# Kernel tuning notes

Hardware: AMD Instinct MI355X
Metric: run time of the kernel (lower is better)

The kernel has to match this reference:

```python
import jax, jax.numpy as jnp
import numpy as np
import math

B, T, D, H = 4, 2048, 1024, 16
DH = D // H

def setup_inputs() -> dict:
    key = jax.random.key(0)
    ks = jax.random.split(key, 5)
    scale = 1.0 / math.sqrt(D)
    x = jax.random.normal(ks[0], (B, T, D), dtype=jnp.float32)
    Wq = jax.random.normal(ks[1], (D, D), dtype=jnp.float32) * scale
    Wk = jax.random.normal(ks[2], (D, D), dtype=jnp.float32) * scale
    Wv = jax.random.normal(ks[3], (D, D), dtype=jnp.float32) * scale
    Wo = jax.random.normal(ks[4], (D, D), dtype=jnp.float32) * scale
    mask = jnp.tril(jnp.ones((T, T), dtype=jnp.int32))  # causal, 1=keep
    return {"x": x, "mask": mask, "Wq": Wq, "Wk": Wk, "Wv": Wv, "Wo": Wo}

def reference(x, mask, Wq, Wk, Wv, Wo):
    Bx, Tx, Dx = x.shape
    # nn.Linear(bias=False): y = x @ W.T
    q = (x @ Wq.T).reshape(Bx, Tx, H, DH).transpose(0, 2, 1, 3)  # [B,H,T,dh]
    k = (x @ Wk.T).reshape(Bx, Tx, H, DH).transpose(0, 2, 1, 3)
    v = (x @ Wv.T).reshape(Bx, Tx, H, DH).transpose(0, 2, 1, 3)
    scores = jnp.einsum('bhqd,bhkd->bhqk', q, k) / math.sqrt(DH)
    m = mask[None, None, :, :]  # [1,1,T,T]
    scores = scores + (m == 0).astype(scores.dtype) * -1e9
    attn = jax.nn.softmax(scores, axis=-1)  # stable (max-subtract) like original
    out = jnp.einsum('bhqk,bhkd->bhqd', attn, v)
    out = out.transpose(0, 2, 1, 3).reshape(Bx, Tx, Dx)
    return out @ Wo.T
```

## Files before the change

kernel.cpp:

```cpp
#include <hip/hip_runtime.h>
#include <stdint.h>

#define B_  4
#define T_  2048
#define D_  1024
#define H_  16
#define DH_ 64

typedef unsigned short u16;
typedef __attribute__((ext_vector_type(8))) short bf16x8;
typedef __attribute__((ext_vector_type(8))) unsigned short u16x8;
typedef __attribute__((ext_vector_type(4))) unsigned short u16x4;
typedef __attribute__((ext_vector_type(4))) float f32x4;

#define NT_ ((size_t)B_ * T_ * D_)
#define QSCALE 0.18033688011112043f

__device__ __forceinline__ u16 f2bf(float f) {
    union { float f; uint32_t u; } v; v.f = f;
    uint32_t r = v.u + 0x7FFFu + ((v.u >> 16) & 1u);
    return (u16)(r >> 16);
}

__device__ __forceinline__ uint32_t pack2(float lo, float hi) {
    union { float f; uint32_t u; } a, b; a.f = lo; b.f = hi;
    return __builtin_amdgcn_perm(b.u, a.u, 0x07060302u);
}

__device__ __forceinline__ void gl2lds16(const u16* g, u16* l) {
    __builtin_amdgcn_global_load_lds(
        (const __attribute__((address_space(1))) unsigned int*)g,
        (__attribute__((address_space(3))) unsigned int*)l,
        16, 0, 0);
}

#define VMCNT(n) asm volatile("s_waitcnt vmcnt(" #n ")" ::: "memory")
#define LGKM0()  asm volatile("s_waitcnt lgkmcnt(0)" ::: "memory")
#define SB0()    __builtin_amdgcn_sched_barrier(0)

__device__ __forceinline__ bf16x8 ldsrd(const u16* base, int row, int ks,
                                        int lq, int swzr) {
    int off = row * 128 + ks * 64 + lq * 16;
    return *(const bf16x8*)((const char*)base + (off ^ swzr));
}

__global__ __launch_bounds__(256) void cvt_x_kernel(
    const float* __restrict__ src, u16* __restrict__ dst, int n8)
{
    int i = blockIdx.x * 256 + threadIdx.x;
    if (i >= n8) return;
    f32x4 a = ((const f32x4*)src)[2 * i];
    f32x4 b = ((const f32x4*)src)[2 * i + 1];
    u16x8 o;
    o[0]=f2bf(a[0]); o[1]=f2bf(a[1]); o[2]=f2bf(a[2]); o[3]=f2bf(a[3]);
    o[4]=f2bf(b[0]); o[5]=f2bf(b[1]); o[6]=f2bf(b[2]); o[7]=f2bf(b[3]);
    ((u16x8*)dst)[i] = o;
}

__global__ __launch_bounds__(256) void cvt_w_kernel(
    const float* __restrict__ w0, const float* __restrict__ w1,
    const float* __restrict__ w2, const float* __restrict__ w3,
    u16* __restrict__ dst)
{
    const float* src = (blockIdx.y == 0) ? w0 : (blockIdx.y == 1) ? w1
                     : (blockIdx.y == 2) ? w2 : w3;
    u16* d = dst + (size_t)blockIdx.y * (D_ * D_);
    int i = blockIdx.x * 256 + threadIdx.x;
    f32x4 a = ((const f32x4*)src)[2 * i];
    f32x4 b = ((const f32x4*)src)[2 * i + 1];
    u16x8 o;
    o[0]=f2bf(a[0]); o[1]=f2bf(a[1]); o[2]=f2bf(a[2]); o[3]=f2bf(a[3]);
    o[4]=f2bf(b[0]); o[5]=f2bf(b[1]); o[6]=f2bf(b[2]); o[7]=f2bf(b[3]);
    ((u16x8*)d)[i] = o;
}

template<int OUT_MODE>
__global__ __launch_bounds__(512) void gemm8_kernel(
    const u16* __restrict__ X, const u16* __restrict__ W,
    void* __restrict__ C, int M, int N, int K)
{
    __shared__ __align__(16) u16 Ab2[2][256 * 64];
    __shared__ __align__(16) u16 Bb2[2][192 * 64];

    const int tid  = threadIdx.x;
    const int wave = tid >> 6;
    const int lane = tid & 63;
    const int lq = lane >> 4, lm = lane & 15;
    const int wm = wave >> 2;
    const int wn = wave & 3;

    const int xcd = (int)blockIdx.x & 7;
    const int idx = (int)blockIdx.x >> 3;
    const int m0 = (((xcd & 3) << 3) + (idx & 7)) << 8;
    const int n0 = (((xcd >> 2) << 3) + (idx >> 3)) * 192;

    const int srow = wave * 8 + (lane >> 3);
    const int scol = ((lane & 7) ^ (lane >> 3)) << 3;
    const u16* gA = X + (size_t)(m0 + srow) * K + scol;
    const u16* gB = W + (size_t)(n0 + srow) * K + scol;
    const size_t rK64 = (size_t)64 * K;

    const int swzr = (lm & 7) << 4;

    f32x4 acc[8][3] = {};
    const int NT = K >> 6;

    gl2lds16(gA,            (u16*)Ab2[0] + wave * 512);
    gl2lds16(gA + rK64,     (u16*)Ab2[0] + 4096  + wave * 512);
    gl2lds16(gA + 2 * rK64, (u16*)Ab2[0] + 8192  + wave * 512);
    gl2lds16(gA + 3 * rK64, (u16*)Ab2[0] + 12288 + wave * 512);
    gl2lds16(gB,            (u16*)Bb2[0] + wave * 512);
    gl2lds16(gB + rK64,     (u16*)Bb2[0] + 4096  + wave * 512);
    gl2lds16(gB + 2 * rK64, (u16*)Bb2[0] + 8192  + wave * 512);
    gl2lds16(gB + 64,            (u16*)Bb2[1] + wave * 512);
    gl2lds16(gB + 64 + rK64,     (u16*)Bb2[1] + 4096  + wave * 512);
    gl2lds16(gB + 64 + 2 * rK64, (u16*)Bb2[1] + 8192  + wave * 512);
    VMCNT(3);
    __builtin_amdgcn_s_barrier();

#define MFMA_HALF(IOFF)                                                     \
        __builtin_amdgcn_s_setprio(1);                                      \
        _Pragma("unroll")                                                   \
        for (int ks = 0; ks < 2; ++ks)                                      \
            _Pragma("unroll")                                               \
            for (int i4 = 0; i4 < 4; ++i4)                                  \
                _Pragma("unroll")                                           \
                for (int j = 0; j < 3; ++j)                                 \
                    acc[(IOFF) + i4][j] =                                   \
                        __builtin_amdgcn_mfma_f32_16x16x32_bf16(            \
                            af[i4][ks], bq[j][ks], acc[(IOFF) + i4][j],     \
                            0, 0, 0);                                       \
        __builtin_amdgcn_s_setprio(0);

#pragma unroll 1
    for (int t = 0; t < NT; ++t) {
        const u16* Ac = Ab2[t & 1];
        const u16* Bc = Bb2[t & 1];
        u16* Abn = (u16*)Ab2[(t + 1) & 1];
        u16* Bbc = (u16*)Bb2[t & 1];
        const bool stA = (t + 1 < NT);
        const bool stB = (t + 2 < NT);
        const u16* gAs = gA + (size_t)(t + 1) * 64;
        const u16* gBs = gB + (size_t)(t + 2) * 64;

        bf16x8 af[4][2], bq[3][2];

#pragma unroll
        for (int i4 = 0; i4 < 4; ++i4)
#pragma unroll
            for (int ks = 0; ks < 2; ++ks)
                af[i4][ks] = ldsrd(Ac, wm * 128 + i4 * 16 + lm, ks, lq, swzr);
#pragma unroll
        for (int j = 0; j < 3; ++j)
#pragma unroll
            for (int ks = 0; ks < 2; ++ks)
                bq[j][ks] = ldsrd(Bc, wn * 48 + j * 16 + lm, ks, lq, swzr);
        if (stA) {
            gl2lds16(gAs,        Abn + wave * 512);
            gl2lds16(gAs + rK64, Abn + 4096 + wave * 512);
        }
        SB0(); __builtin_amdgcn_s_barrier();
        LGKM0(); SB0();
        MFMA_HALF(0)
        SB0(); __builtin_amdgcn_s_barrier();

#pragma unroll
        for (int i4 = 0; i4 < 4; ++i4)
#pragma unroll
            for (int ks = 0; ks < 2; ++ks)
                af[i4][ks] = ldsrd(Ac, wm * 128 + (4 + i4) * 16 + lm, ks, lq, swzr);
        if (stA) {
            gl2lds16(gAs + 2 * rK64, Abn + 8192  + wave * 512);
            gl2lds16(gAs + 3 * rK64, Abn + 12288 + wave * 512);
        }
        if (stB) {
            gl2lds16(gBs,            Bbc + wave * 512);
            gl2lds16(gBs + rK64,     Bbc + 4096 + wave * 512);
            gl2lds16(gBs + 2 * rK64, Bbc + 8192 + wave * 512);
        }
        SB0(); __builtin_amdgcn_s_barrier();
        LGKM0(); SB0();
        MFMA_HALF(4)
        SB0();
        if (stB)      { VMCNT(3); }
        else if (stA) { VMCNT(0); }
        __builtin_amdgcn_s_barrier();
    }
#undef MFMA_HALF

#pragma unroll
    for (int i = 0; i < 8; ++i)
#pragma unroll
        for (int j = 0; j < 3; ++j) {
            int rowb = m0 + wm * 128 + i * 16 + lq * 4;
            int col  = n0 + wn * 48 + j * 16 + lm;
            if (OUT_MODE == 2) {
#pragma unroll
                for (int r = 0; r < 4; ++r)
                    ((float*)C)[(size_t)(rowb + r) * N + col] = acc[i][j][r];
            } else {
                u16* Qp = (u16*)C;
                int region = col >> 10;
                int colr = col & 1023;
                if (region == 0) {
#pragma unroll
                    for (int r = 0; r < 4; ++r)
                        Qp[(size_t)(rowb + r) * D_ + colr] = f2bf(acc[i][j][r] * QSCALE);
                } else if (region == 1) {
#pragma unroll
                    for (int r = 0; r < 4; ++r)
                        (Qp + NT_)[(size_t)(rowb + r) * D_ + colr] = f2bf(acc[i][j][r]);
                } else {
                    int b = rowb >> 11, tt2 = rowb & (T_ - 1);
                    u16x4 pk;
#pragma unroll
                    for (int r = 0; r < 4; ++r) pk[r] = f2bf(acc[i][j][r]);
                    *(u16x4*)((Qp + 2 * NT_) + ((size_t)b * D_ + colr) * T_ + tt2) = pk;
                }
            }
        }
}

__global__ __launch_bounds__(512) void gemm8o_kernel(
    const u16* __restrict__ X, const u16* __restrict__ W,
    float* __restrict__ C)
{
    __shared__ __align__(16) u16 Ab2[2][256 * 64];
    __shared__ __align__(16) u16 Bb2[2][128 * 64];

    const int K = 1024, N = 1024;
    const int tid  = threadIdx.x;
    const int wave = tid >> 6;
    const int lane = tid & 63;
    const int lq = lane >> 4, lm = lane & 15;
    const int wm = wave >> 2;
    const int wn = wave & 3;

    const int xcd = (int)blockIdx.x & 7;
    const int idx = (int)blockIdx.x >> 3;
    const int m0 = (((xcd & 3) << 3) + (idx & 7)) << 8;
    const int n0 = (((xcd >> 2) << 2) + (idx >> 3)) << 7;

    const int srow = wave * 8 + (lane >> 3);
    const int scol = ((lane & 7) ^ (lane >> 3)) << 3;
    const u16* gA = X + (size_t)(m0 + srow) * K + scol;
    const u16* gB = W + (size_t)(n0 + srow) * K + scol;
    const size_t rK64 = (size_t)64 * K;

    const int swzr = (lm & 7) << 4;

    f32x4 acc[8][2] = {};
    bf16x8 afA[2][2], afB[2][2];
    bf16x8 bqA[2][2], bqB[2][2];
    const int NT = 16;

    gl2lds16(gA,            (u16*)Ab2[0] + wave * 512);
    gl2lds16(gA + rK64,     (u16*)Ab2[0] + 4096  + wave * 512);
    gl2lds16(gA + 2 * rK64, (u16*)Ab2[0] + 8192  + wave * 512);
    gl2lds16(gA + 3 * rK64, (u16*)Ab2[0] + 12288 + wave * 512);
    gl2lds16(gB,            (u16*)Bb2[0] + wave * 512);
    gl2lds16(gB + rK64,     (u16*)Bb2[0] + 4096  + wave * 512);
    gl2lds16(gB + 64,            (u16*)Bb2[1] + wave * 512);
    gl2lds16(gB + 64 + rK64,     (u16*)Bb2[1] + 4096  + wave * 512);
    VMCNT(2);
    __builtin_amdgcn_s_barrier();
#pragma unroll
    for (int i2 = 0; i2 < 2; ++i2)
#pragma unroll
        for (int ks = 0; ks < 2; ++ks)
            afA[i2][ks] = ldsrd(Ab2[0], wm * 128 + i2 * 16 + lm, ks, lq, swzr);
#pragma unroll
    for (int j = 0; j < 2; ++j)
#pragma unroll
        for (int ks = 0; ks < 2; ++ks)
            bqA[j][ks] = ldsrd(Bb2[0], wn * 32 + j * 16 + lm, ks, lq, swzr);

    auto tile_body = [&](int t, bf16x8 (&bqU)[2][2], bf16x8 (&bqF)[2][2])
        __attribute__((always_inline)) -> void {
        const u16* Ac = Ab2[t & 1];
        const u16* An = Ab2[(t + 1) & 1];
        const u16* Bn = Bb2[(t + 1) & 1];
        u16* Abn = (u16*)Ab2[(t + 1) & 1];
        u16* Bbc = (u16*)Bb2[t & 1];
        const bool stA = (t + 1 < NT);
        const bool stB = (t + 2 < NT);
        const u16* gAs = gA + (size_t)(t + 1) * 64;
        const u16* gBs = gB + (size_t)(t + 2) * 64;

#define MFMA_PHO(Q, AF, BQ)                                                 \
        __builtin_amdgcn_s_setprio(1);                                      \
        _Pragma("unroll")                                                   \
        for (int ks = 0; ks < 2; ++ks)                                      \
            _Pragma("unroll")                                               \
            for (int i2 = 0; i2 < 2; ++i2)                                  \
                _Pragma("unroll")                                           \
                for (int j = 0; j < 2; ++j)                                 \
                    acc[2 * (Q) + i2][j] =                                  \
                        __builtin_amdgcn_mfma_f32_16x16x32_bf16(            \
                            AF[i2][ks], BQ[j][ks], acc[2 * (Q) + i2][j],    \
                            0, 0, 0);                                       \
        __builtin_amdgcn_s_setprio(0);

#define RD_AFO(SET, P, BASE)                                                \
        _Pragma("unroll")                                                   \
        for (int i2 = 0; i2 < 2; ++i2)                                      \
            _Pragma("unroll")                                               \
            for (int ks = 0; ks < 2; ++ks)                                  \
                SET[i2][ks] = ldsrd(BASE,                                   \
                    wm * 128 + (2 * (P) + i2) * 16 + lm, ks, lq, swzr);

        RD_AFO(afB, 1, Ac);
        if (stA) {
            gl2lds16(gAs,        Abn + wave * 512);
            gl2lds16(gAs + rK64, Abn + 4096 + wave * 512);
        }
        SB0(); __builtin_amdgcn_s_barrier(); SB0();
        MFMA_PHO(0, afA, bqU); SB0();
        __builtin_amdgcn_s_barrier();

        RD_AFO(afA, 2, Ac);
        if (stA) {
            gl2lds16(gAs + 2 * rK64, Abn + 8192  + wave * 512);
            gl2lds16(gAs + 3 * rK64, Abn + 12288 + wave * 512);
        }
        SB0(); __builtin_amdgcn_s_barrier(); SB0();
        MFMA_PHO(1, afB, bqU); SB0();
        __builtin_amdgcn_s_barrier();

        RD_AFO(afB, 3, Ac);
        if (stB)
            gl2lds16(gBs, Bbc + wave * 512);
        SB0(); __builtin_amdgcn_s_barrier(); SB0();
        MFMA_PHO(2, afA, bqU); SB0();
        if (stB)      { VMCNT(1); }
        else if (stA) { VMCNT(0); }
        __builtin_amdgcn_s_barrier();

        if (stA) {
            RD_AFO(afA, 0, An);
#pragma unroll
            for (int j = 0; j < 2; ++j)
#pragma unroll
                for (int ks = 0; ks < 2; ++ks)
                    bqF[j][ks] = ldsrd(Bn, wn * 32 + j * 16 + lm, ks, lq, swzr);
        }
        if (stB)
            gl2lds16(gBs + rK64, Bbc + 4096 + wave * 512);
        SB0(); __builtin_amdgcn_s_barrier(); SB0();
        MFMA_PHO(3, afB, bqU); SB0();
        __builtin_amdgcn_s_barrier();
#undef RD_AFO
#undef MFMA_PHO
    };

#pragma unroll 1
    for (int tt = 0; tt < NT; tt += 2) {
        tile_body(tt,     bqA, bqB);
        tile_body(tt + 1, bqB, bqA);
    }

#pragma unroll
    for (int i = 0; i < 8; ++i)
#pragma unroll
        for (int j = 0; j < 2; ++j) {
            int rowb = m0 + wm * 128 + i * 16 + lq * 4;
            int col  = n0 + wn * 32 + j * 16 + lm;
#pragma unroll
            for (int r = 0; r < 4; ++r)
                C[(size_t)(rowb + r) * N + col] = acc[i][j][r];
        }
}

__global__ __launch_bounds__(128) void attn_kernel(
    const u16* __restrict__ Qg, const u16* __restrict__ Kg,
    const u16* __restrict__ Vtg, u16* __restrict__ Og)
{
    __shared__ __align__(16) u16 Pl[2 * 64 * 40];

    const int tid  = threadIdx.x;
    const int wave = tid >> 6;
    const int lane = tid & 63;
    const int lq = lane >> 4, lm = lane & 15;
    const int id = blockIdx.x;
    const int xs = id & 7;
    const int bh = xs + 8 * ((id >> 3) & 7);
    const int qj = 31 - (id >> 6);
    const int b = bh >> 4, h = bh & 15;

    const size_t batchoff = (size_t)b * T_ * D_;
    const size_t headoff  = (size_t)h * DH_;
    const size_t vbase    = (size_t)bh * DH_ * T_;

    u16* pw = Pl + wave * 64 * 40;

    const int qw  = qj * 64;
    const int ktd = qj >> 1;
    const int odd = qj & 1;

    bf16x8 aq[4][2];
#pragma unroll
    for (int qf = 0; qf < 4; ++qf) {
        const u16* qrow = Qg + batchoff + (size_t)(qw + qf * 16 + lm) * D_ + headoff;
        aq[qf][0] = *(const bf16x8*)(qrow + lq * 8);
        aq[qf][1] = *(const bf16x8*)(qrow + 32 + lq * 8);
    }

    f32x4 oaccT[4][4] = {};
    float l_lane[4] = {0.f, 0.f, 0.f, 0.f};

#pragma unroll 1
    for (int kt = wave; kt <= ktd; kt += 2) {
        const bool diag = (kt == ktd);
        const int ksmax = diag ? (odd ? 3 : 1) : 3;

#pragma unroll
        for (int c = 0; c < 4; ++c) {
            if (c <= ksmax) {
#pragma unroll
                for (int t = 0; t < 2; ++t) {
                    const int mt = 2 * c + t;
                    const u16* krow = Kg + batchoff
                        + (size_t)(kt * 128 + mt * 16 + lm) * D_ + headoff;
                    bf16x8 kf0 = *(const bf16x8*)(krow + lq * 8);
                    bf16x8 kf1 = *(const bf16x8*)(krow + 32 + lq * 8);
                    f32x4 s[4];
                    __builtin_amdgcn_s_setprio(1);
#pragma unroll
                    for (int qf = 0; qf < 4; ++qf) {
                        s[qf] = f32x4{0.f, 0.f, 0.f, 0.f};
                        s[qf] = __builtin_amdgcn_mfma_f32_16x16x32_bf16(
                            kf0, aq[qf][0], s[qf], 0, 0, 0);
                        s[qf] = __builtin_amdgcn_mfma_f32_16x16x32_bf16(
                            kf1, aq[qf][1], s[qf], 0, 0, 0);
                    }
                    __builtin_amdgcn_s_setprio(0);
                    if (diag) {
                        int keyb = kt * 128 + mt * 16 + lq * 4;
#pragma unroll
                        for (int qf = 0; qf < 4; ++qf) {
                            int query = qw + qf * 16 + lm;
#pragma unroll
                            for (int r = 0; r < 4; ++r)
                                if (keyb + r > query) s[qf][r] = -1e9f;
                        }
                    }
#pragma unroll
                    for (int qf = 0; qf < 4; ++qf) {
                        float p0 = __builtin_amdgcn_exp2f(s[qf][0]);
                        float p1 = __builtin_amdgcn_exp2f(s[qf][1]);
                        float p2 = __builtin_amdgcn_exp2f(s[qf][2]);
                        float p3 = __builtin_amdgcn_exp2f(s[qf][3]);
                        l_lane[qf] += (p0 + p1) + (p2 + p3);
                        uint2 d; d.x = pack2(p0, p1); d.y = pack2(p2, p3);
                        *(uint2*)(pw + (qf * 16 + lm) * 40 + t * 16 + lq * 4) = d;
                    }
                }

                bf16x8 pf[4];
#pragma unroll
                for (int qf = 0; qf < 4; ++qf)
                    pf[qf] = *(const bf16x8*)(pw + (qf * 16 + lm) * 40 + lq * 8);
                __builtin_amdgcn_s_setprio(1);
#pragma unroll
                for (int mo = 0; mo < 4; ++mo) {
                    const u16* vrow = Vtg + vbase
                        + (size_t)(mo * 16 + lm) * T_ + kt * 128 + c * 32;
                    bf16x8 vf = *(const bf16x8*)(vrow + lq * 8);
#pragma unroll
                    for (int qf = 0; qf < 4; ++qf)
                        oaccT[qf][mo] = __builtin_amdgcn_mfma_f32_16x16x32_bf16(
                            vf, pf[qf], oaccT[qf][mo], 0, 0, 0);
                }
                __builtin_amdgcn_s_setprio(0);
            }
        }
    }

    float* Cf = (float*)Pl;
    const int cswz = (lane ^ (lane >> 3)) * 4;
    __syncthreads();
    if (wave == 1) {
#pragma unroll
        for (int qf = 0; qf < 2; ++qf)
#pragma unroll
            for (int mo = 0; mo < 4; ++mo)
                *(f32x4*)&Cf[(qf * 4 + mo) * 256 + cswz] = oaccT[qf][mo];
#pragma unroll
        for (int qf = 0; qf < 4; ++qf)
            Cf[2048 + qf * 64 + lane] = l_lane[qf];
    }
    __syncthreads();
    if (wave == 0) {
#pragma unroll
        for (int qf = 0; qf < 2; ++qf)
#pragma unroll
            for (int mo = 0; mo < 4; ++mo) {
                f32x4 o = *(const f32x4*)&Cf[(qf * 4 + mo) * 256 + cswz];
#pragma unroll
                for (int r = 0; r < 4; ++r) oaccT[qf][mo][r] += o[r];
            }
#pragma unroll
        for (int qf = 0; qf < 4; ++qf) l_lane[qf] += Cf[2048 + qf * 64 + lane];
    }
    __syncthreads();
    if (wave == 1) {
#pragma unroll
        for (int qf = 2; qf < 4; ++qf)
#pragma unroll
            for (int mo = 0; mo < 4; ++mo)
                *(f32x4*)&Cf[((qf - 2) * 4 + mo) * 256 + cswz] = oaccT[qf][mo];
    }
    __syncthreads();
    if (wave == 0) {
#pragma unroll
        for (int qf = 2; qf < 4; ++qf)
#pragma unroll
            for (int mo = 0; mo < 4; ++mo) {
                f32x4 o = *(const f32x4*)&Cf[((qf - 2) * 4 + mo) * 256 + cswz];
#pragma unroll
                for (int r = 0; r < 4; ++r) oaccT[qf][mo][r] += o[r];
            }
#pragma unroll
        for (int qf = 0; qf < 4; ++qf) {
            float l = l_lane[qf];
            l += __shfl_xor(l, 16, 64);
            l += __shfl_xor(l, 32, 64);
            float inv = 1.0f / l;
            int row = qw + qf * 16 + lm;
            u16* obase = Og + batchoff + (size_t)row * D_ + headoff;
#pragma unroll
            for (int mo = 0; mo < 4; ++mo) {
                uint2 d;
                d.x = pack2(oaccT[qf][mo][0] * inv, oaccT[qf][mo][1] * inv);
                d.y = pack2(oaccT[qf][mo][2] * inv, oaccT[qf][mo][3] * inv);
                *(uint2*)(obase + mo * 16 + lq * 4) = d;
            }
        }
    }
}

extern "C" void kernel_launch(void* const* d_in, const int* in_sizes, int n_in,
                              void* d_out, int out_size, void* d_ws, size_t ws_size,
                              hipStream_t stream)
{
    const float* x  = (const float*)d_in[0];
    const float* Wq = (const float*)d_in[2];
    const float* Wk = (const float*)d_in[3];
    const float* Wv = (const float*)d_in[4];
    const float* Wo = (const float*)d_in[5];

    const size_t DD = (size_t)D_ * D_;
    u16* Qb  = (u16*)d_ws;
    u16* Kb  = Qb + NT_;
    u16* Vb  = Kb + NT_;
    u16* Ob  = Vb + NT_;
    u16* xb  = Ob + NT_;
    u16* wb  = xb + NT_;

    const int M = B_ * T_;

    cvt_x_kernel<<<dim3((int)(NT_ / 8 / 256)), 256, 0, stream>>>(x, xb, (int)(NT_ / 8));
    cvt_w_kernel<<<dim3((int)(DD / 8 / 256), 4), 256, 0, stream>>>(Wq, Wk, Wv, Wo, wb);

    gemm8_kernel<3><<<dim3((M / 256) * (3 * D_ / 192)), 512, 0, stream>>>(
        xb, wb, Qb, M, 3 * D_, D_);

    attn_kernel<<<dim3(2048), 128, 0, stream>>>(Qb, Kb, Vb, Ob);

    gemm8o_kernel<<<dim3(256), 512, 0, stream>>>(Ob, wb + 3 * DD, (float*)d_out);
}
```

Baseline: 268.8 us.

## Merge GEMM K-step halves into one phase with triple-buffered B tiles

The projection GEMM main loop used to split each 64-wide K tile into two halves, each with its own LDS reads, global-to-LDS prefetches and block barrier. It now reads all eight A fragments at once, issues every A and B prefetch together, and runs all 48 MFMAs in one burst, leaving a single barrier per iteration. The B tile buffer becomes a three-slot ring, so the tile two steps ahead can be loaded without overwriting the one being read. The aim is to halve barrier stalls per K step. In exchange it uses more LDS and more VGPRs for the A fragments, and it overlaps LDS reads with MFMAs less finely.

Measured after the change: 267.4 us. About the same (-0.5%).

```diff
diff --git a/kernel.cpp b/kernel.cpp
--- a/kernel.cpp
+++ b/kernel.cpp
@@ -80,7 +80,7 @@
     void* __restrict__ C, int M, int N, int K)
 {
     __shared__ __align__(16) u16 Ab2[2][256 * 64];
-    __shared__ __align__(16) u16 Bb2[2][192 * 64];
+    __shared__ __align__(16) u16 Bb3[3][192 * 64];
 
     const int tid  = threadIdx.x;
     const int wave = tid >> 6;
@@ -109,84 +109,68 @@
     gl2lds16(gA + rK64,     (u16*)Ab2[0] + 4096  + wave * 512);
     gl2lds16(gA + 2 * rK64, (u16*)Ab2[0] + 8192  + wave * 512);
     gl2lds16(gA + 3 * rK64, (u16*)Ab2[0] + 12288 + wave * 512);
-    gl2lds16(gB,            (u16*)Bb2[0] + wave * 512);
-    gl2lds16(gB + rK64,     (u16*)Bb2[0] + 4096  + wave * 512);
-    gl2lds16(gB + 2 * rK64, (u16*)Bb2[0] + 8192  + wave * 512);
-    gl2lds16(gB + 64,            (u16*)Bb2[1] + wave * 512);
-    gl2lds16(gB + 64 + rK64,     (u16*)Bb2[1] + 4096  + wave * 512);
-    gl2lds16(gB + 64 + 2 * rK64, (u16*)Bb2[1] + 8192  + wave * 512);
+    gl2lds16(gB,            (u16*)Bb3[0] + wave * 512);
+    gl2lds16(gB + rK64,     (u16*)Bb3[0] + 4096  + wave * 512);
+    gl2lds16(gB + 2 * rK64, (u16*)Bb3[0] + 8192  + wave * 512);
+    gl2lds16(gB + 64,            (u16*)Bb3[1] + wave * 512);
+    gl2lds16(gB + 64 + rK64,     (u16*)Bb3[1] + 4096  + wave * 512);
+    gl2lds16(gB + 64 + 2 * rK64, (u16*)Bb3[1] + 8192  + wave * 512);
     VMCNT(3);
     __builtin_amdgcn_s_barrier();
 
-#define MFMA_HALF(IOFF)                                                     \
-        __builtin_amdgcn_s_setprio(1);                                      \
-        _Pragma("unroll")                                                   \
-        for (int ks = 0; ks < 2; ++ks)                                      \
-            _Pragma("unroll")                                               \
-            for (int i4 = 0; i4 < 4; ++i4)                                  \
-                _Pragma("unroll")                                           \
-                for (int j = 0; j < 3; ++j)                                 \
-                    acc[(IOFF) + i4][j] =                                   \
-                        __builtin_amdgcn_mfma_f32_16x16x32_bf16(            \
-                            af[i4][ks], bq[j][ks], acc[(IOFF) + i4][j],     \
-                            0, 0, 0);                                       \
-        __builtin_amdgcn_s_setprio(0);
-
+    int bc = 0;
 #pragma unroll 1
     for (int t = 0; t < NT; ++t) {
         const u16* Ac = Ab2[t & 1];
-        const u16* Bc = Bb2[t & 1];
+        const u16* Bc = Bb3[bc];
         u16* Abn = (u16*)Ab2[(t + 1) & 1];
-        u16* Bbc = (u16*)Bb2[t & 1];
+        int bs = bc + 2; if (bs >= 3) bs -= 3;
+        u16* Bbs = (u16*)Bb3[bs];
         const bool stA = (t + 1 < NT);
         const bool stB = (t + 2 < NT);
         const u16* gAs = gA + (size_t)(t + 1) * 64;
         const u16* gBs = gB + (size_t)(t + 2) * 64;
 
-        bf16x8 af[4][2], bq[3][2];
-
-#pragma unroll
-        for (int i4 = 0; i4 < 4; ++i4)
+        bf16x8 af[8][2], bq[3][2];
+#pragma unroll
+        for (int i = 0; i < 8; ++i)
 #pragma unroll
             for (int ks = 0; ks < 2; ++ks)
-                af[i4][ks] = ldsrd(Ac, wm * 128 + i4 * 16 + lm, ks, lq, swzr);
+                af[i][ks] = ldsrd(Ac, wm * 128 + i * 16 + lm, ks, lq, swzr);
 #pragma unroll
         for (int j = 0; j < 3; ++j)
 #pragma unroll
             for (int ks = 0; ks < 2; ++ks)
                 bq[j][ks] = ldsrd(Bc, wn * 48 + j * 16 + lm, ks, lq, swzr);
         if (stA) {
-            gl2lds16(gAs,        Abn + wave * 512);
-            gl2lds16(gAs + rK64, Abn + 4096 + wave * 512);
+            gl2lds16(gAs,            Abn + wave * 512);
+            gl2lds16(gAs + rK64,     Abn + 4096  + wave * 512);
+            gl2lds16(gAs + 2 * rK64, Abn + 8192  + wave * 512);
+            gl2lds16(gAs + 3 * rK64, Abn + 12288 + wave * 512);
+        }
+        if (stB) {
+            gl2lds16(gBs,            Bbs + wave * 512);
+            gl2lds16(gBs + rK64,     Bbs + 4096 + wave * 512);
+            gl2lds16(gBs + 2 * rK64, Bbs + 8192 + wave * 512);
         }
         SB0(); __builtin_amdgcn_s_barrier();
         LGKM0(); SB0();
-        MFMA_HALF(0)
-        SB0(); __builtin_amdgcn_s_barrier();
-
-#pragma unroll
-        for (int i4 = 0; i4 < 4; ++i4)
-#pragma unroll
-            for (int ks = 0; ks < 2; ++ks)
-                af[i4][ks] = ldsrd(Ac, wm * 128 + (4 + i4) * 16 + lm, ks, lq, swzr);
-        if (stA) {
-            gl2lds16(gAs + 2 * rK64, Abn + 8192  + wave * 512);
-            gl2lds16(gAs + 3 * rK64, Abn + 12288 + wave * 512);
-        }
-        if (stB) {
-            gl2lds16(gBs,            Bbc + wave * 512);
-            gl2lds16(gBs + rK64,     Bbc + 4096 + wave * 512);
-            gl2lds16(gBs + 2 * rK64, Bbc + 8192 + wave * 512);
-        }
-        SB0(); __builtin_amdgcn_s_barrier();
-        LGKM0(); SB0();
-        MFMA_HALF(4)
+        __builtin_amdgcn_s_setprio(1);
+#pragma unroll
+        for (int ks = 0; ks < 2; ++ks)
+#pragma unroll
+            for (int i = 0; i < 8; ++i)
+#pragma unroll
+                for (int j = 0; j < 3; ++j)
+                    acc[i][j] = __builtin_amdgcn_mfma_f32_16x16x32_bf16(
+                        af[i][ks], bq[j][ks], acc[i][j], 0, 0, 0);
+        __builtin_amdgcn_s_setprio(0);
         SB0();
         if (stB)      { VMCNT(3); }
         else if (stA) { VMCNT(0); }
         __builtin_amdgcn_s_barrier();
-    }
-#undef MFMA_HALF
+        ++bc; if (bc == 3) bc = 0;
+    }
 
 #pragma unroll
     for (int i = 0; i < 8; ++i)
@@ -295,7 +279,7 @@
             for (int i2 = 0; i2 < 2; ++i2)                                  \
                 _Pragma("unroll")                                           \
                 for (int j = 0; j < 2; ++j)                                 \
-                    acc[2 * (Q) + i2][j] =                                  \
+                    acc[2 * (Q) + i2][j] =                                   \
                         __builtin_amdgcn_mfma_f32_16x16x32_bf16(            \
                             AF[i2][ks], BQ[j][ks], acc[2 * (Q) + i2][j],    \
                             0, 0, 0);                                       \
```
